# Performance work log

Hardware: AMD Instinct MI355X
Metric: run time of the kernel (lower is better)

## Reference

```python
import jax, jax.numpy as jnp
import numpy as np

DIM = 384
HEADS = 12
WIN = (4, 4, 4)
SHIFT = (2, 2, 2)
N_TOK = WIN[0] * WIN[1] * WIN[2]  # 64
MLP_HIDDEN = 4 * DIM
TABLE = (2 * WIN[0] - 1) * (2 * WIN[1] - 1) * (2 * WIN[2] - 1)  # 343
EPS = 1e-5


def _rel_pos_index():
    d, h, w = WIN
    coords = np.stack(np.meshgrid(np.arange(d), np.arange(h), np.arange(w), indexing='ij'))
    cf = coords.reshape(3, -1)                      # (3, n)
    rel = (cf[:, :, None] - cf[:, None, :]).transpose(1, 2, 0)  # (n, n, 3)
    idx = ((rel[..., 0] + d - 1) * ((2 * h - 1) * (2 * w - 1))
           + (rel[..., 1] + h - 1) * (2 * w - 1)
           + (rel[..., 2] + w - 1))
    return jnp.asarray(idx, dtype=jnp.int32)        # (n, n)


def setup_inputs() -> dict:
    key = jax.random.key(0)
    ks = jax.random.split(key, 8)
    s = 0.02
    return {
        'x': jax.random.normal(ks[0], (1, 16, 64, 64, DIM), dtype=jnp.float32),
        'ln1_g': jnp.ones((DIM,), jnp.float32),
        'ln1_b': jnp.zeros((DIM,), jnp.float32),
        'qkv_w': jax.random.normal(ks[1], (DIM, 3 * DIM), jnp.float32) * s,
        'qkv_b': jnp.zeros((3 * DIM,), jnp.float32),
        'rpb_table': jax.random.normal(ks[2], (TABLE, HEADS), jnp.float32) * s,
        'proj_w': jax.random.normal(ks[3], (DIM, DIM), jnp.float32) * s,
        'proj_b': jnp.zeros((DIM,), jnp.float32),
        'ln2_g': jnp.ones((DIM,), jnp.float32),
        'ln2_b': jnp.zeros((DIM,), jnp.float32),
        'mlp_w1': jax.random.normal(ks[4], (DIM, MLP_HIDDEN), jnp.float32) * s,
        'mlp_b1': jnp.zeros((MLP_HIDDEN,), jnp.float32),
        'mlp_w2': jax.random.normal(ks[5], (MLP_HIDDEN, DIM), jnp.float32) * s,
        'mlp_b2': jnp.zeros((DIM,), jnp.float32),
    }


def _layernorm(t, g, b):
    mu = jnp.mean(t, axis=-1, keepdims=True)
    var = jnp.mean(jnp.square(t - mu), axis=-1, keepdims=True)
    return (t - mu) * jax.lax.rsqrt(var + EPS) * g + b


def reference(x, ln1_g, ln1_b, qkv_w, qkv_b, rpb_table, proj_w, proj_b,
              ln2_g, ln2_b, mlp_w1, mlp_b1, mlp_w2, mlp_b2):
    b, d, h, w, c = x.shape
    dw, hw, ww = WIN
    hd = c // HEADS
    scale = hd ** -0.5

    y = _layernorm(x, ln1_g, ln1_b)
    y = jnp.roll(y, (-SHIFT[0], -SHIFT[1], -SHIFT[2]), axis=(1, 2, 3))

    # window partition: (b, d, h, w, c) -> (b*nW, n_tok, c)
    y = y.reshape(b, d // dw, dw, h // hw, hw, w // ww, ww, c)
    y = y.transpose(0, 1, 3, 5, 2, 4, 6, 7).reshape(-1, N_TOK, c)

    qkv = (y @ qkv_w + qkv_b).reshape(-1, N_TOK, 3, HEADS, hd)
    qkv = qkv.transpose(2, 0, 3, 1, 4)              # (3, B_, H, n, hd)
    q, k, v = qkv[0] * scale, qkv[1], qkv[2]

    attn = jnp.einsum('bhnd,bhmd->bhnm', q, k)      # (B_, H, n, n)
    bias = rpb_table[_rel_pos_index()]              # (n, n, H)
    attn = attn + bias.transpose(2, 0, 1)[None]
    attn = jax.nn.softmax(attn, axis=-1)

    o = jnp.einsum('bhnm,bhmd->bhnd', attn, v)
    o = o.transpose(0, 2, 1, 3).reshape(-1, N_TOK, c)
    o = o @ proj_w + proj_b

    # window reverse: (b*nW, n_tok, c) -> (b, d, h, w, c)
    o = o.reshape(b, d // dw, h // hw, w // ww, dw, hw, ww, c)
    o = o.transpose(0, 1, 4, 2, 5, 3, 6, 7).reshape(b, d, h, w, c)
    o = jnp.roll(o, SHIFT, axis=(1, 2, 3))

    x = x + o
    y2 = _layernorm(x, ln2_g, ln2_b)
    y2 = jax.nn.gelu(y2 @ mlp_w1 + mlp_b1, approximate=False) @ mlp_w2 + mlp_b2
    return x + y2
```

## Files before the change

### kernel.cpp

```cpp
#include <hip/hip_runtime.h>
#include <math.h>

#define DIM 384
#define HEADS 12
#define MTOT 65536

typedef _Float16 f16;
typedef f16 f16x8 __attribute__((ext_vector_type(8)));
typedef float f32x4 __attribute__((ext_vector_type(4)));

typedef const __attribute__((address_space(1))) unsigned int* gas1;
typedef __attribute__((address_space(3))) unsigned int* las3;

template<bool GATHER>
__global__ __launch_bounds__(128)
void ln_kernel(const float* __restrict__ x, const float* __restrict__ g,
               const float* __restrict__ b, f16* __restrict__ y)
{
    int r = blockIdx.x;
    size_t src;
    if (GATHER) {
        int win = r >> 6, tok = r & 63;
        int wd = win >> 8, wh = (win >> 4) & 15, ww = win & 15;
        int zd = tok >> 4, zh = (tok >> 2) & 3, zw = tok & 3;
        int d = ((wd << 2) + zd + 2) & 15;
        int h = ((wh << 2) + zh + 2) & 63;
        int w = ((ww << 2) + zw + 2) & 63;
        src = (size_t)((((d << 6) + h) << 6) + w);
    } else {
        src = (size_t)r;
    }
    const float* xr = x + src * (size_t)DIM;
    int t = threadIdx.x;
    float v0 = xr[t], v1 = xr[t + 128], v2 = xr[t + 256];
    float s  = v0 + v1 + v2;
    float ss = v0 * v0 + v1 * v1 + v2 * v2;
    #pragma unroll
    for (int off = 32; off > 0; off >>= 1) {
        s  += __shfl_down(s, off);
        ss += __shfl_down(ss, off);
    }
    __shared__ float sm[4];
    if ((t & 63) == 0) { sm[t >> 6] = s; sm[2 + (t >> 6)] = ss; }
    __syncthreads();
    float S = sm[0] + sm[1], SS = sm[2] + sm[3];
    float mu  = S * (1.0f / DIM);
    float var = SS * (1.0f / DIM) - mu * mu;
    float rs  = rsqrtf(var + 1e-5f);
    f16* yr = y + (size_t)r * DIM;
    yr[t]       = (f16)((v0 - mu) * rs * g[t]       + b[t]);
    yr[t + 128] = (f16)((v1 - mu) * rs * g[t + 128] + b[t + 128]);
    yr[t + 256] = (f16)((v2 - mu) * rs * g[t + 256] + b[t + 256]);
}

__global__ __launch_bounds__(128)
void wcvt_kernel(const float* __restrict__ W, f16* __restrict__ Wt, int N, int K)
{
    int k = blockIdx.x * 128 + threadIdx.x;
    int n = blockIdx.y;
    Wt[(size_t)n * K + k] = (f16)W[(size_t)k * N + n];
}

__device__ __forceinline__ void stage_pair(const f16* __restrict__ Ag, const f16* __restrict__ Bg,
                                           f16* Asb, f16* Bsb, int K, int kt, int wv, int lane)
{
    #pragma unroll
    for (int i = 0; i < 2; ++i) {
        int r  = wv * 32 + i * 16 + (lane >> 2);
        int c  = lane & 3;
        int gc = c ^ ((r >> 1) & 3);
        const f16* ga = Ag + (size_t)r * K + kt * 32 + gc * 8;
        const f16* gb = Bg + (size_t)r * K + kt * 32 + gc * 8;
        __builtin_amdgcn_global_load_lds((gas1)ga, (las3)(Asb + r * 32 + c * 8), 16, 0, 0);
        __builtin_amdgcn_global_load_lds((gas1)gb, (las3)(Bsb + r * 32 + c * 8), 16, 0, 0);
    }
}

template<int EPI>
__global__ __launch_bounds__(256)
void gemm_kernel(const f16* __restrict__ A, const f16* __restrict__ Wt,
                 const float* __restrict__ bias, const float* __restrict__ res,
                 void* __restrict__ outv, int N, int K)
{
    __shared__ f16 As[3][128 * 32];
    __shared__ f16 Bs[3][128 * 32];
    int tid = threadIdx.x;
    int lane = tid & 63, wv = tid >> 6;
    int bm = blockIdx.y << 7, bn = blockIdx.x << 7;
    int fr = lane & 15, fq = lane >> 4;
    int wr = wv >> 1, wc = wv & 1;

    const f16* Ag = A  + (size_t)bm * K;
    const f16* Bg = Wt + (size_t)bn * K;

    f32x4 zero4 = {0.f, 0.f, 0.f, 0.f};
    f32x4 acc[4][4];
    #pragma unroll
    for (int i = 0; i < 4; ++i)
        #pragma unroll
        for (int j = 0; j < 4; ++j) acc[i][j] = zero4;

    int nk = K >> 5;
    stage_pair(Ag, Bg, As[0], Bs[0], K, 0, wv, lane);
    stage_pair(Ag, Bg, As[1], Bs[1], K, 1, wv, lane);
    int cur = 0;
    for (int t = 0; t < nk; ++t) {
        if (t + 1 < nk) asm volatile("s_waitcnt vmcnt(4)" ::: "memory");
        else            asm volatile("s_waitcnt vmcnt(0)" ::: "memory");
        __builtin_amdgcn_s_barrier();
        if (t + 2 < nk) {
            int nxt = cur + 2; if (nxt >= 3) nxt -= 3;
            stage_pair(Ag, Bg, As[nxt], Bs[nxt], K, t + 2, wv, lane);
        }
        f16x8 a[4], b[4];
        #pragma unroll
        for (int i = 0; i < 4; ++i) {
            int R  = wr * 64 + i * 16 + fr;
            int Nn = wc * 64 + i * 16 + fr;
            a[i] = *(const f16x8*)&As[cur][R  * 32 + (fq ^ ((R  >> 1) & 3)) * 8];
            b[i] = *(const f16x8*)&Bs[cur][Nn * 32 + (fq ^ ((Nn >> 1) & 3)) * 8];
        }
        __builtin_amdgcn_s_setprio(1);
        #pragma unroll
        for (int i = 0; i < 4; ++i)
            #pragma unroll
            for (int j = 0; j < 4; ++j)
                acc[i][j] = __builtin_amdgcn_mfma_f32_16x16x32_f16(a[i], b[j], acc[i][j], 0, 0, 0);
        __builtin_amdgcn_s_setprio(0);
        cur = (cur == 2) ? 0 : cur + 1;
    }

    #pragma unroll
    for (int i = 0; i < 4; ++i) {
        int mrow = bm + wr * 64 + i * 16 + fq * 4;
        #pragma unroll
        for (int j = 0; j < 4; ++j) {
            int n = bn + wc * 64 + j * 16 + fr;
            float bi = bias[n];
            #pragma unroll
            for (int r = 0; r < 4; ++r) {
                int m = mrow + r;
                float v = acc[i][j][r] + bi;
                if constexpr (EPI == 0) {
                    ((f16*)outv)[(size_t)m * N + n] = (f16)v;
                } else if constexpr (EPI == 1) {
                    v = 0.5f * v * (1.0f + erff(v * 0.70710678118654752f));
                    ((f16*)outv)[(size_t)m * N + n] = (f16)v;
                } else if constexpr (EPI == 2) {
                    int win = m >> 6, tok = m & 63;
                    int wd = win >> 8, wh = (win >> 4) & 15, ww = win & 15;
                    int zd = tok >> 4, zh = (tok >> 2) & 3, zw = tok & 3;
                    int d = ((wd << 2) + zd + 2) & 15;
                    int h = ((wh << 2) + zh + 2) & 63;
                    int w = ((ww << 2) + zw + 2) & 63;
                    size_t orow = (size_t)((((d << 6) + h) << 6) + w);
                    ((float*)outv)[orow * DIM + n] = v + res[orow * DIM + n];
                } else {
                    ((float*)outv)[(size_t)m * DIM + n] = v + res[(size_t)m * DIM + n];
                }
            }
        }
    }
}

__global__ __launch_bounds__(64)
void attn_kernel(const f16* __restrict__ qkv, const float* __restrict__ rpb,
                 f16* __restrict__ o)
{
    __shared__ f16 P[64][72];
    __shared__ f16 Vt[32][72];
    int win = blockIdx.x, head = blockIdx.y;
    int lane = threadIdx.x;
    int fr = lane & 15, fq = lane >> 4;
    const float scale = 0.17677669529663687f;
    const f16* qb = qkv + (size_t)win * 64 * 1152 + head * 32;

    f16x8 qf[4], kf[4];
    #pragma unroll
    for (int i = 0; i < 4; ++i) {
        qf[i] = *(const f16x8*)(qb + (size_t)(i * 16 + fr) * 1152 + fq * 8);
        kf[i] = *(const f16x8*)(qb + (size_t)(i * 16 + fr) * 1152 + DIM + fq * 8);
    }
    {
        const f16* vb = qb + (size_t)lane * 1152 + 2 * DIM;
        #pragma unroll
        for (int c = 0; c < 4; ++c) {
            f16x8 vv = *(const f16x8*)(vb + c * 8);
            #pragma unroll
            for (int e = 0; e < 8; ++e) Vt[c * 8 + e][lane] = vv[e];
        }
    }

    f32x4 zero4 = {0.f, 0.f, 0.f, 0.f};
    f32x4 s[4][4];
    #pragma unroll
    for (int i = 0; i < 4; ++i)
        #pragma unroll
        for (int j = 0; j < 4; ++j) s[i][j] = zero4;
    #pragma unroll
    for (int i = 0; i < 4; ++i)
        #pragma unroll
        for (int j = 0; j < 4; ++j)
            s[i][j] = __builtin_amdgcn_mfma_f32_16x16x32_f16(qf[i], kf[j], s[i][j], 0, 0, 0);

    #pragma unroll
    for (int i = 0; i < 4; ++i) {
        #pragma unroll
        for (int r = 0; r < 4; ++r) {
            int zq = i * 16 + fq * 4 + r;
            int zd = zq >> 4, zh = (zq >> 2) & 3, zw = zq & 3;
            float tv[4];
            float mx = -1e30f;
            #pragma unroll
            for (int j = 0; j < 4; ++j) {
                int m = j * 16 + fr;
                int md = m >> 4, mh = (m >> 2) & 3, mw = m & 3;
                int idx = (zd - md + 3) * 49 + (zh - mh + 3) * 7 + (zw - mw + 3);
                float v = s[i][j][r] * scale + rpb[idx * HEADS + head];
                tv[j] = v;
                mx = fmaxf(mx, v);
            }
            mx = fmaxf(mx, __shfl_xor(mx, 1));
            mx = fmaxf(mx, __shfl_xor(mx, 2));
            mx = fmaxf(mx, __shfl_xor(mx, 4));
            mx = fmaxf(mx, __shfl_xor(mx, 8));
            float sum = 0.f;
            #pragma unroll
            for (int j = 0; j < 4; ++j) { tv[j] = expf(tv[j] - mx); sum += tv[j]; }
            sum += __shfl_xor(sum, 1);
            sum += __shfl_xor(sum, 2);
            sum += __shfl_xor(sum, 4);
            sum += __shfl_xor(sum, 8);
            float is = 1.0f / sum;
            #pragma unroll
            for (int j = 0; j < 4; ++j) P[zq][j * 16 + fr] = (f16)(tv[j] * is);
        }
    }
    __syncthreads();

    f32x4 oacc[4][2];
    #pragma unroll
    for (int i = 0; i < 4; ++i)
        #pragma unroll
        for (int jd = 0; jd < 2; ++jd) oacc[i][jd] = zero4;
    #pragma unroll
    for (int i = 0; i < 4; ++i)
        #pragma unroll
        for (int jd = 0; jd < 2; ++jd)
            #pragma unroll
            for (int ks = 0; ks < 2; ++ks) {
                f16x8 pa = *(const f16x8*)&P[i * 16 + fr][ks * 32 + fq * 8];
                f16x8 vb = *(const f16x8*)&Vt[jd * 16 + fr][ks * 32 + fq * 8];
                oacc[i][jd] = __builtin_amdgcn_mfma_f32_16x16x32_f16(pa, vb, oacc[i][jd], 0, 0, 0);
            }
    #pragma unroll
    for (int i = 0; i < 4; ++i)
        #pragma unroll
        for (int jd = 0; jd < 2; ++jd)
            #pragma unroll
            for (int r = 0; r < 4; ++r)
                o[(size_t)(win * 64 + i * 16 + fq * 4 + r) * DIM + head * 32 + jd * 16 + fr]
                    = (f16)oacc[i][jd][r];
}

extern "C" void kernel_launch(void* const* d_in, const int* in_sizes, int n_in,
                              void* d_out, int out_size, void* d_ws, size_t ws_size,
                              hipStream_t stream)
{
    const float* x      = (const float*)d_in[0];
    const float* ln1_g  = (const float*)d_in[1];
    const float* ln1_b  = (const float*)d_in[2];
    const float* qkv_w  = (const float*)d_in[3];
    const float* qkv_b  = (const float*)d_in[4];
    const float* rpb    = (const float*)d_in[5];
    const float* proj_w = (const float*)d_in[6];
    const float* proj_b = (const float*)d_in[7];
    const float* ln2_g  = (const float*)d_in[8];
    const float* ln2_b  = (const float*)d_in[9];
    const float* mlp_w1 = (const float*)d_in[10];
    const float* mlp_b1 = (const float*)d_in[11];
    const float* mlp_w2 = (const float*)d_in[12];
    const float* mlp_b2 = (const float*)d_in[13];
    float* out = (float*)d_out;

    f16* wq = (f16*)d_ws;
    f16* wp = wq + 1152 * 384;
    f16* w1 = wp + 384 * 384;
    f16* w2 = w1 + 1536 * 384;
    f16* Yh = w2 + 384 * 1536;
    f16* CH = Yh + (size_t)MTOT * DIM;
    size_t used_halves = (size_t)1769472 + (size_t)MTOT * DIM;
    size_t ws_halves = ws_size / 2;
    size_t remh = ws_halves > used_halves ? ws_halves - used_halves : 0;
    int rows_chunk = 1024;
    for (int rc = MTOT; rc >= 1024; rc >>= 1)
        if ((size_t)rc * 1536 <= remh) { rows_chunk = rc; break; }

    wcvt_kernel<<<dim3(3, 1152), 128, 0, stream>>>(qkv_w, wq, 1152, 384);
    wcvt_kernel<<<dim3(3, 384),  128, 0, stream>>>(proj_w, wp, 384, 384);
    wcvt_kernel<<<dim3(3, 1536), 128, 0, stream>>>(mlp_w1, w1, 1536, 384);
    wcvt_kernel<<<dim3(12, 384), 128, 0, stream>>>(mlp_w2, w2, 384, 1536);

    ln_kernel<true><<<MTOT, 128, 0, stream>>>(x, ln1_g, ln1_b, Yh);

    for (int r0 = 0; r0 < MTOT; r0 += rows_chunk) {
        gemm_kernel<0><<<dim3(9, rows_chunk / 128), 256, 0, stream>>>(
            Yh + (size_t)r0 * DIM, wq, qkv_b, nullptr, CH, 1152, 384);
        attn_kernel<<<dim3(rows_chunk / 64, HEADS), 64, 0, stream>>>(
            CH, rpb, Yh + (size_t)r0 * DIM);
    }

    gemm_kernel<2><<<dim3(3, MTOT / 128), 256, 0, stream>>>(
        Yh, wp, proj_b, x, out, 384, 384);

    ln_kernel<false><<<MTOT, 128, 0, stream>>>(out, ln2_g, ln2_b, Yh);

    for (int r0 = 0; r0 < MTOT; r0 += rows_chunk) {
        gemm_kernel<1><<<dim3(12, rows_chunk / 128), 256, 0, stream>>>(
            Yh + (size_t)r0 * DIM, w1, mlp_b1, nullptr, CH, 1536, 384);
        gemm_kernel<3><<<dim3(3, rows_chunk / 128), 256, 0, stream>>>(
            CH, w2, mlp_b2, out + (size_t)r0 * DIM, out + (size_t)r0 * DIM, 384, 1536);
    }
}
```

Baseline: 801.5 us.

## Fuse QKV projection with window attention and fuse the two MLP GEMMs

Replaces the QKV GEMM plus separate attention kernel with one per-window kernel that computes Q/K/V for head pairs from LDS-resident LN output and runs attention in place. It also fuses MLP fc1+GELU+fc2 into one kernel that keeps the hidden tile in LDS and accumulates the fc2 output in registers. This removes the large QKV and hidden-activation round trips through global memory and several launches. In exchange, weights are read directly from global memory without LDS staging, fewer blocks are launched, and LDS use per block is high, which may limit occupancy and MFMA throughput.

Result: slower. 1.019 ms (+27.2%).

```diff
diff --git a/kernel.cpp b/kernel.cpp
--- a/kernel.cpp
+++ b/kernel.cpp
@@ -76,11 +76,10 @@
     }
 }
 
-template<int EPI>
 __global__ __launch_bounds__(256)
 void gemm_kernel(const f16* __restrict__ A, const f16* __restrict__ Wt,
                  const float* __restrict__ bias, const float* __restrict__ res,
-                 void* __restrict__ outv, int N, int K)
+                 float* __restrict__ outv, int N, int K)
 {
     __shared__ f16 As[3][128 * 32];
     __shared__ f16 Bs[3][128 * 32];
@@ -140,127 +139,239 @@
             #pragma unroll
             for (int r = 0; r < 4; ++r) {
                 int m = mrow + r;
-                float v = acc[i][j][r] + bi;
-                if constexpr (EPI == 0) {
-                    ((f16*)outv)[(size_t)m * N + n] = (f16)v;
-                } else if constexpr (EPI == 1) {
-                    v = 0.5f * v * (1.0f + erff(v * 0.70710678118654752f));
-                    ((f16*)outv)[(size_t)m * N + n] = (f16)v;
-                } else if constexpr (EPI == 2) {
-                    int win = m >> 6, tok = m & 63;
-                    int wd = win >> 8, wh = (win >> 4) & 15, ww = win & 15;
-                    int zd = tok >> 4, zh = (tok >> 2) & 3, zw = tok & 3;
-                    int d = ((wd << 2) + zd + 2) & 15;
-                    int h = ((wh << 2) + zh + 2) & 63;
-                    int w = ((ww << 2) + zw + 2) & 63;
-                    size_t orow = (size_t)((((d << 6) + h) << 6) + w);
-                    ((float*)outv)[orow * DIM + n] = v + res[orow * DIM + n];
-                } else {
-                    ((float*)outv)[(size_t)m * DIM + n] = v + res[(size_t)m * DIM + n];
-                }
-            }
-        }
-    }
-}
-
-__global__ __launch_bounds__(64)
-void attn_kernel(const f16* __restrict__ qkv, const float* __restrict__ rpb,
-                 f16* __restrict__ o)
-{
+                int win = m >> 6, tok = m & 63;
+                int wd = win >> 8, wh = (win >> 4) & 15, ww = win & 15;
+                int zd = tok >> 4, zh = (tok >> 2) & 3, zw = tok & 3;
+                int d = ((wd << 2) + zd + 2) & 15;
+                int h = ((wh << 2) + zh + 2) & 63;
+                int w = ((ww << 2) + zw + 2) & 63;
+                size_t orow = (size_t)((((d << 6) + h) << 6) + w);
+                outv[orow * DIM + n] = acc[i][j][r] + bi + res[orow * DIM + n];
+            }
+        }
+    }
+}
+
+__global__ __launch_bounds__(256)
+void fqa_kernel(f16* __restrict__ Yh, const f16* __restrict__ wt,
+                const float* __restrict__ qbias, const float* __restrict__ rpb)
+{
+    __shared__ f16 y_s[64][392];
+    __shared__ f16 q_s[2][64][40];
+    __shared__ f16 k_s[2][64][40];
+    __shared__ f16 vt_s[2][32][72];
     __shared__ f16 P[64][72];
-    __shared__ f16 Vt[32][72];
-    int win = blockIdx.x, head = blockIdx.y;
-    int lane = threadIdx.x;
+    int win = blockIdx.x;
+    int tid = threadIdx.x, lane = tid & 63, wv = tid >> 6;
     int fr = lane & 15, fq = lane >> 4;
     const float scale = 0.17677669529663687f;
-    const f16* qb = qkv + (size_t)win * 64 * 1152 + head * 32;
-
-    f16x8 qf[4], kf[4];
-    #pragma unroll
-    for (int i = 0; i < 4; ++i) {
-        qf[i] = *(const f16x8*)(qb + (size_t)(i * 16 + fr) * 1152 + fq * 8);
-        kf[i] = *(const f16x8*)(qb + (size_t)(i * 16 + fr) * 1152 + DIM + fq * 8);
-    }
+    f16* yg = Yh + (size_t)win * 64 * DIM;
+
     {
-        const f16* vb = qb + (size_t)lane * 1152 + 2 * DIM;
-        #pragma unroll
-        for (int c = 0; c < 4; ++c) {
-            f16x8 vv = *(const f16x8*)(vb + c * 8);
-            #pragma unroll
-            for (int e = 0; e < 8; ++e) Vt[c * 8 + e][lane] = vv[e];
-        }
-    }
+        int row = tid >> 2, c0 = (tid & 3) * 96;
+        #pragma unroll
+        for (int i = 0; i < 12; ++i)
+            *(f16x8*)&y_s[row][c0 + i * 8] = *(const f16x8*)(yg + row * DIM + c0 + i * 8);
+    }
+    __syncthreads();
 
     f32x4 zero4 = {0.f, 0.f, 0.f, 0.f};
-    f32x4 s[4][4];
+    for (int hp = 0; hp < 6; ++hp) {
+        f32x4 acc[3][4];
+        #pragma unroll
+        for (int jn = 0; jn < 3; ++jn)
+            #pragma unroll
+            for (int i = 0; i < 4; ++i) acc[jn][i] = zero4;
+        #pragma unroll
+        for (int kk = 0; kk < 12; ++kk) {
+            f16x8 a[4];
+            #pragma unroll
+            for (int i = 0; i < 4; ++i)
+                a[i] = *(const f16x8*)&y_s[i * 16 + fr][kk * 32 + fq * 8];
+            #pragma unroll
+            for (int jn = 0; jn < 3; ++jn) {
+                int nf = wv * 3 + jn;
+                int which = nf >> 1, tp = which >> 1, hh = which & 1;
+                int gcol = tp * 384 + (hp * 2 + hh) * 32 + (nf & 1) * 16 + fr;
+                f16x8 b = *(const f16x8*)(wt + (size_t)gcol * 384 + kk * 32 + fq * 8);
+                #pragma unroll
+                for (int i = 0; i < 4; ++i)
+                    acc[jn][i] = __builtin_amdgcn_mfma_f32_16x16x32_f16(a[i], b, acc[jn][i], 0, 0, 0);
+            }
+        }
+        #pragma unroll
+        for (int jn = 0; jn < 3; ++jn) {
+            int nf = wv * 3 + jn;
+            int which = nf >> 1, tp = which >> 1, hh = which & 1;
+            int colhd = (nf & 1) * 16 + fr;
+            float bi = qbias[tp * 384 + (hp * 2 + hh) * 32 + colhd];
+            #pragma unroll
+            for (int i = 0; i < 4; ++i)
+                #pragma unroll
+                for (int r = 0; r < 4; ++r) {
+                    int row = i * 16 + fq * 4 + r;
+                    float v = acc[jn][i][r] + bi;
+                    if (tp == 0)      q_s[hh][row][colhd] = (f16)(v * scale);
+                    else if (tp == 1) k_s[hh][row][colhd] = (f16)v;
+                    else              vt_s[hh][colhd][row] = (f16)v;
+                }
+        }
+        __syncthreads();
+
+        #pragma unroll
+        for (int hh = 0; hh < 2; ++hh) {
+            int head = hp * 2 + hh;
+            f16x8 qf = *(const f16x8*)&q_s[hh][wv * 16 + fr][fq * 8];
+            f32x4 s[4];
+            #pragma unroll
+            for (int j = 0; j < 4; ++j) {
+                f16x8 kf = *(const f16x8*)&k_s[hh][j * 16 + fr][fq * 8];
+                s[j] = __builtin_amdgcn_mfma_f32_16x16x32_f16(qf, kf, zero4, 0, 0, 0);
+            }
+            #pragma unroll
+            for (int r = 0; r < 4; ++r) {
+                int zq = wv * 16 + fq * 4 + r;
+                int zd = zq >> 4, zh = (zq >> 2) & 3, zw = zq & 3;
+                float tv[4];
+                float mx = -1e30f;
+                #pragma unroll
+                for (int j = 0; j < 4; ++j) {
+                    int m = j * 16 + fr;
+                    int md = m >> 4, mh = (m >> 2) & 3, mw = m & 3;
+                    int idx = (zd - md + 3) * 49 + (zh - mh + 3) * 7 + (zw - mw + 3);
+                    float v = s[j][r] + rpb[idx * HEADS + head];
+                    tv[j] = v;
+                    mx = fmaxf(mx, v);
+                }
+                mx = fmaxf(mx, __shfl_xor(mx, 1));
+                mx = fmaxf(mx, __shfl_xor(mx, 2));
+                mx = fmaxf(mx, __shfl_xor(mx, 4));
+                mx = fmaxf(mx, __shfl_xor(mx, 8));
+                float sum = 0.f;
+                #pragma unroll
+                for (int j = 0; j < 4; ++j) { tv[j] = expf(tv[j] - mx); sum += tv[j]; }
+                sum += __shfl_xor(sum, 1);
+                sum += __shfl_xor(sum, 2);
+                sum += __shfl_xor(sum, 4);
+                sum += __shfl_xor(sum, 8);
+                float is = 1.0f / sum;
+                #pragma unroll
+                for (int j = 0; j < 4; ++j) P[zq][j * 16 + fr] = (f16)(tv[j] * is);
+            }
+            f32x4 oacc[2] = {zero4, zero4};
+            #pragma unroll
+            for (int jd = 0; jd < 2; ++jd)
+                #pragma unroll
+                for (int ks = 0; ks < 2; ++ks) {
+                    f16x8 pa = *(const f16x8*)&P[wv * 16 + fr][ks * 32 + fq * 8];
+                    f16x8 vb = *(const f16x8*)&vt_s[hh][jd * 16 + fr][ks * 32 + fq * 8];
+                    oacc[jd] = __builtin_amdgcn_mfma_f32_16x16x32_f16(pa, vb, oacc[jd], 0, 0, 0);
+                }
+            #pragma unroll
+            for (int jd = 0; jd < 2; ++jd)
+                #pragma unroll
+                for (int r = 0; r < 4; ++r)
+                    yg[(size_t)(wv * 16 + fq * 4 + r) * DIM + head * 32 + jd * 16 + fr]
+                        = (f16)oacc[jd][r];
+        }
+        __syncthreads();
+    }
+}
+
+__global__ __launch_bounds__(512)
+void fmlp_kernel(const f16* __restrict__ Yh, const f16* __restrict__ w1t,
+                 const f16* __restrict__ w2t, const float* __restrict__ b1,
+                 const float* __restrict__ b2, float* __restrict__ outp)
+{
+    __shared__ f16 y_s[128][392];
+    __shared__ f16 hid_s[128][136];
+    int tid = threadIdx.x, lane = tid & 63, wv = tid >> 6;
+    int fr = lane & 15, fq = lane >> 4;
+    int bm = blockIdx.x << 7;
+
+    {
+        int row = tid >> 2, c0 = (tid & 3) * 96;
+        const f16* yg = Yh + (size_t)(bm + row) * DIM + c0;
+        #pragma unroll
+        for (int i = 0; i < 12; ++i)
+            *(f16x8*)&y_s[row][c0 + i * 8] = *(const f16x8*)(yg + i * 8);
+    }
+    __syncthreads();
+
+    int m0a = (wv >> 1) << 5, n0a = (wv & 1) << 6;
+    int m0b = (wv >> 2) << 6, n0b = (wv & 3) * 96;
+
+    f32x4 zero4 = {0.f, 0.f, 0.f, 0.f};
+    f32x4 acc2[4][6];
     #pragma unroll
     for (int i = 0; i < 4; ++i)
         #pragma unroll
-        for (int j = 0; j < 4; ++j) s[i][j] = zero4;
+        for (int j = 0; j < 6; ++j) acc2[i][j] = zero4;
+
+    for (int ht = 0; ht < 12; ++ht) {
+        f32x4 acc1[2][4];
+        #pragma unroll
+        for (int im = 0; im < 2; ++im)
+            #pragma unroll
+            for (int jn = 0; jn < 4; ++jn) acc1[im][jn] = zero4;
+        #pragma unroll
+        for (int kk = 0; kk < 12; ++kk) {
+            f16x8 a[2];
+            #pragma unroll
+            for (int im = 0; im < 2; ++im)
+                a[im] = *(const f16x8*)&y_s[m0a + im * 16 + fr][kk * 32 + fq * 8];
+            #pragma unroll
+            for (int jn = 0; jn < 4; ++jn) {
+                int nh = ht * 128 + n0a + jn * 16 + fr;
+                f16x8 b = *(const f16x8*)(w1t + (size_t)nh * 384 + kk * 32 + fq * 8);
+                #pragma unroll
+                for (int im = 0; im < 2; ++im)
+                    acc1[im][jn] = __builtin_amdgcn_mfma_f32_16x16x32_f16(a[im], b, acc1[im][jn], 0, 0, 0);
+            }
+        }
+        __syncthreads();
+        #pragma unroll
+        for (int im = 0; im < 2; ++im)
+            #pragma unroll
+            for (int jn = 0; jn < 4; ++jn) {
+                float bi = b1[ht * 128 + n0a + jn * 16 + fr];
+                #pragma unroll
+                for (int r = 0; r < 4; ++r) {
+                    float v = acc1[im][jn][r] + bi;
+                    v = 0.5f * v * (1.0f + erff(v * 0.70710678118654752f));
+                    hid_s[m0a + im * 16 + fq * 4 + r][n0a + jn * 16 + fr] = (f16)v;
+                }
+            }
+        __syncthreads();
+        #pragma unroll
+        for (int ks = 0; ks < 4; ++ks) {
+            f16x8 a[4];
+            #pragma unroll
+            for (int i = 0; i < 4; ++i)
+                a[i] = *(const f16x8*)&hid_s[m0b + i * 16 + fr][ks * 32 + fq * 8];
+            #pragma unroll
+            for (int j = 0; j < 6; ++j) {
+                int n = n0b + j * 16 + fr;
+                f16x8 b = *(const f16x8*)(w2t + (size_t)n * 1536 + ht * 128 + ks * 32 + fq * 8);
+                #pragma unroll
+                for (int i = 0; i < 4; ++i)
+                    acc2[i][j] = __builtin_amdgcn_mfma_f32_16x16x32_f16(a[i], b, acc2[i][j], 0, 0, 0);
+            }
+        }
+    }
     #pragma unroll
     for (int i = 0; i < 4; ++i)
         #pragma unroll
-        for (int j = 0; j < 4; ++j)
-            s[i][j] = __builtin_amdgcn_mfma_f32_16x16x32_f16(qf[i], kf[j], s[i][j], 0, 0, 0);
-
-    #pragma unroll
-    for (int i = 0; i < 4; ++i) {
-        #pragma unroll
-        for (int r = 0; r < 4; ++r) {
-            int zq = i * 16 + fq * 4 + r;
-            int zd = zq >> 4, zh = (zq >> 2) & 3, zw = zq & 3;
-            float tv[4];
-            float mx = -1e30f;
-            #pragma unroll
-            for (int j = 0; j < 4; ++j) {
-                int m = j * 16 + fr;
-                int md = m >> 4, mh = (m >> 2) & 3, mw = m & 3;
-                int idx = (zd - md + 3) * 49 + (zh - mh + 3) * 7 + (zw - mw + 3);
-                float v = s[i][j][r] * scale + rpb[idx * HEADS + head];
-                tv[j] = v;
-                mx = fmaxf(mx, v);
-            }
-            mx = fmaxf(mx, __shfl_xor(mx, 1));
-            mx = fmaxf(mx, __shfl_xor(mx, 2));
-            mx = fmaxf(mx, __shfl_xor(mx, 4));
-            mx = fmaxf(mx, __shfl_xor(mx, 8));
-            float sum = 0.f;
-            #pragma unroll
-            for (int j = 0; j < 4; ++j) { tv[j] = expf(tv[j] - mx); sum += tv[j]; }
-            sum += __shfl_xor(sum, 1);
-            sum += __shfl_xor(sum, 2);
-            sum += __shfl_xor(sum, 4);
-            sum += __shfl_xor(sum, 8);
-            float is = 1.0f / sum;
-            #pragma unroll
-            for (int j = 0; j < 4; ++j) P[zq][j * 16 + fr] = (f16)(tv[j] * is);
-        }
-    }
-    __syncthreads();
-
-    f32x4 oacc[4][2];
-    #pragma unroll
-    for (int i = 0; i < 4; ++i)
-        #pragma unroll
-        for (int jd = 0; jd < 2; ++jd) oacc[i][jd] = zero4;
-    #pragma unroll
-    for (int i = 0; i < 4; ++i)
-        #pragma unroll
-        for (int jd = 0; jd < 2; ++jd)
-            #pragma unroll
-            for (int ks = 0; ks < 2; ++ks) {
-                f16x8 pa = *(const f16x8*)&P[i * 16 + fr][ks * 32 + fq * 8];
-                f16x8 vb = *(const f16x8*)&Vt[jd * 16 + fr][ks * 32 + fq * 8];
-                oacc[i][jd] = __builtin_amdgcn_mfma_f32_16x16x32_f16(pa, vb, oacc[i][jd], 0, 0, 0);
-            }
-    #pragma unroll
-    for (int i = 0; i < 4; ++i)
-        #pragma unroll
-        for (int jd = 0; jd < 2; ++jd)
-            #pragma unroll
-            for (int r = 0; r < 4; ++r)
-                o[(size_t)(win * 64 + i * 16 + fq * 4 + r) * DIM + head * 32 + jd * 16 + fr]
-                    = (f16)oacc[i][jd][r];
+        for (int j = 0; j < 6; ++j) {
+            int n = n0b + j * 16 + fr;
+            float bi = b2[n];
+            #pragma unroll
+            for (int r = 0; r < 4; ++r) {
+                int m = bm + m0b + i * 16 + fq * 4 + r;
+                size_t oidx = (size_t)m * DIM + n;
+                outp[oidx] = acc2[i][j][r] + bi + outp[oidx];
+            }
+        }
 }
 
 extern "C" void kernel_launch(void* const* d_in, const int* in_sizes, int n_in,
@@ -288,13 +399,6 @@
     f16* w1 = wp + 384 * 384;
     f16* w2 = w1 + 1536 * 384;
     f16* Yh = w2 + 384 * 1536;
-    f16* CH = Yh + (size_t)MTOT * DIM;
-    size_t used_halves = (size_t)1769472 + (size_t)MTOT * DIM;
-    size_t ws_halves = ws_size / 2;
-    size_t remh = ws_halves > used_halves ? ws_halves - used_halves : 0;
-    int rows_chunk = 1024;
-    for (int rc = MTOT; rc >= 1024; rc >>= 1)
-        if ((size_t)rc * 1536 <= remh) { rows_chunk = rc; break; }
 
     wcvt_kernel<<<dim3(3, 1152), 128, 0, stream>>>(qkv_w, wq, 1152, 384);
     wcvt_kernel<<<dim3(3, 384),  128, 0, stream>>>(proj_w, wp, 384, 384);
@@ -303,22 +407,12 @@
 
     ln_kernel<true><<<MTOT, 128, 0, stream>>>(x, ln1_g, ln1_b, Yh);
 
-    for (int r0 = 0; r0 < MTOT; r0 += rows_chunk) {
-        gemm_kernel<0><<<dim3(9, rows_chunk / 128), 256, 0, stream>>>(
-            Yh + (size_t)r0 * DIM, wq, qkv_b, nullptr, CH, 1152, 384);
-        attn_kernel<<<dim3(rows_chunk / 64, HEADS), 64, 0, stream>>>(
-            CH, rpb, Yh + (size_t)r0 * DIM);
-    }
-
-    gemm_kernel<2><<<dim3(3, MTOT / 128), 256, 0, stream>>>(
+    fqa_kernel<<<1024, 256, 0, stream>>>(Yh, wq, qkv_b, rpb);
+
+    gemm_kernel<<<dim3(3, MTOT / 128), 256, 0, stream>>>(
         Yh, wp, proj_b, x, out, 384, 384);
 
     ln_kernel<false><<<MTOT, 128, 0, stream>>>(out, ln2_g, ln2_b, Yh);
 
-    for (int r0 = 0; r0 < MTOT; r0 += rows_chunk) {
-        gemm_kernel<1><<<dim3(12, rows_chunk / 128), 256, 0, stream>>>(
-            Yh + (size_t)r0 * DIM, w1, mlp_b1, nullptr, CH, 1536, 384);
-        gemm_kernel<3><<<dim3(3, rows_chunk / 128), 256, 0, stream>>>(
-            CH, w2, mlp_b2, out + (size_t)r0 * DIM, out + (size_t)r0 * DIM, 384, 1536);
-    }
-}
+    fmlp_kernel<<<MTOT / 128, 512, 0, stream>>>(Yh, w1, w2, mlp_b1, mlp_b2, out);
+}
```
